# Optimization experiments

Hardware: AMD Instinct MI355X
Metric: run time of the kernel (lower is better)

## Reference

```python
import jax, jax.numpy as jnp
import numpy as np

B, T, OBS = 16, 4095, 128
HID, NH, FF, NL = 256, 8, 1024, 4
DH = HID // NH
ACT = 32
KEPS = 0.001   # performer kernel_epsilon (generalized attention default)
LNEPS = 1e-6   # flax LayerNorm default eps


def setup_inputs() -> dict:
    key = jax.random.key(0)
    ks = list(jax.random.split(key, 16))
    s = 0.02
    r = lambda k, shape: jax.random.normal(k, shape, jnp.float32) * s
    return {
        "hidden_state": jnp.zeros((B, 1, HID), jnp.float32),
        "ins": jax.random.normal(ks[0], (B, T, OBS), jnp.float32),
        "resets": jax.random.randint(ks[1], (B,), 0, 2).astype(bool),
        "emb_W": r(ks[2], (OBS, HID)), "emb_b": jnp.zeros((HID,), jnp.float32),
        "Wq": r(ks[3], (NL, HID, NH, DH)), "bq": jnp.zeros((NL, NH, DH), jnp.float32),
        "Wk": r(ks[4], (NL, HID, NH, DH)), "bk": jnp.zeros((NL, NH, DH), jnp.float32),
        "Wv": r(ks[5], (NL, HID, NH, DH)), "bv": jnp.zeros((NL, NH, DH), jnp.float32),
        "Wo": r(ks[6], (NL, NH, DH, HID)), "bo": jnp.zeros((NL, HID), jnp.float32),
        "ln1_s": jnp.ones((NL, HID), jnp.float32), "ln1_b": jnp.zeros((NL, HID), jnp.float32),
        "W1": r(ks[7], (NL, HID, FF)), "b1": jnp.zeros((NL, FF), jnp.float32),
        "W2": r(ks[8], (NL, FF, HID)), "b2": jnp.zeros((NL, HID), jnp.float32),
        "ln2_s": jnp.ones((NL, HID), jnp.float32), "ln2_b": jnp.zeros((NL, HID), jnp.float32),
        "qp_W": r(ks[9], (HID, ACT)), "qp_b": jnp.zeros((ACT,), jnp.float32),
    }


def layer_norm(x, scale, bias):
    m = x.mean(-1, keepdims=True)
    v = ((x - m) ** 2).mean(-1, keepdims=True)
    return (x - m) * jax.lax.rsqrt(v + LNEPS) * scale + bias


def favor_attention(q, k, v):
    # FAVOR+ generalized attention with deterministic relu features (no random
    # projection, make_fast_generalized_attention defaults), bidirectional,
    # renormalized. q,k,v: [B, L, H, Dh]; feature dim M == Dh.
    qp = jax.nn.relu(q) + KEPS
    kp = jax.nn.relu(k) + KEPS
    kv = jnp.einsum('blhm,blhd->bhmd', kp, v)            # [B,H,M,Dh]
    num = jnp.einsum('blhm,bhmd->blhd', qp, kv)           # [B,L,H,Dh]
    den = jnp.einsum('blhm,bhm->blh', qp, kp.sum(axis=1))  # [B,L,H]
    return num / den[..., None]


def encoder_block(x, Wq, bq, Wk, bk, Wv, bv, Wo, bo, ln1_s, ln1_b, W1, b1, W2, b2, ln2_s, ln2_b):
    q = jnp.einsum('bld,dhm->blhm', x, Wq) + bq
    k = jnp.einsum('bld,dhm->blhm', x, Wk) + bk
    v = jnp.einsum('bld,dhm->blhm', x, Wv) + bv
    a = favor_attention(q, k, v)
    o = jnp.einsum('blhm,hmd->bld', a, Wo) + bo
    x = o + o  # faithful to source: x = attn(x); x = x + dropout(x)
    x = layer_norm(x, ln1_s, ln1_b)
    h = jax.nn.relu(x @ W1 + b1) @ W2 + b2
    h = h + h  # same residual quirk on the FFN branch
    return layer_norm(h, ln2_s, ln2_b)


def reference(hidden_state, ins, resets, emb_W, emb_b, Wq, bq, Wk, bk, Wv, bv, Wo, bo, ln1_s, ln1_b, W1, b1, W2, b2, ln2_s, ln2_b, qp_W, qp_b):
    emb = ins @ emb_W + emb_b                         # [B, T, HID]
    hs = jnp.where(resets[:, None, None], 0.0, hidden_state)
    x = jnp.concatenate([hs, emb], axis=-2)           # [B, 1+T, HID]
    for i in range(NL):
        x = encoder_block(x, Wq[i], bq[i], Wk[i], bk[i], Wv[i], bv[i], Wo[i], bo[i],
                          ln1_s[i], ln1_b[i], W1[i], b1[i], W2[i], b2[i], ln2_s[i], ln2_b[i])
    new_hidden = x[..., 0:1, :]                       # carry token
    q_vals = new_hidden @ qp_W + qp_b                 # [B, 1, ACT]
    return new_hidden, q_vals
```

## Files before the change

kernel.cpp:

```cpp
#include <hip/hip_runtime.h>


typedef unsigned short bf16_t;
typedef __attribute__((ext_vector_type(8))) short short8;
typedef __attribute__((ext_vector_type(4))) float float4v;

#define NB 16
#define LSEQ 4096
#define MROWS (NB * LSEQ)
#define HIDD 256
#define NHEAD 8
#define DHEAD 32
#define FFD 1024
#define NLAY 4
#define KEPS_F 1e-3f
#define LNEPS_F 1e-6f
#define KV_ELEMS (NB * NHEAD * 32 * 33)

__device__ __forceinline__ float b2f(bf16_t h) {
    return __uint_as_float(((unsigned int)h) << 16);
}
__device__ __forceinline__ bf16_t f2b(float f) {
    unsigned int u = __float_as_uint(f);
    u += 0x7fffu + ((u >> 16) & 1u);
    return (bf16_t)(u >> 16);
}

#define GLOAD_LDS16(g, l)                                                     \
    __builtin_amdgcn_global_load_lds(                                         \
        (const __attribute__((address_space(1))) void*)(g),                   \
        (__attribute__((address_space(3))) void*)(l), 16, 0, 0)

#define SBAR() __builtin_amdgcn_s_barrier()
#define WAITV(n)                                                              \
    do {                                                                      \
        asm volatile("s_waitcnt vmcnt(" #n ")" ::: "memory");                 \
        __builtin_amdgcn_sched_barrier(0);                                    \
    } while (0)

#define FRAG16(L, R)                                                          \
    (*(const short8*)&(L)[((((R) >> 1) * 8) +                                  \
        (((((R) & 1) << 2) | quad) ^ (((R) >> 1) & 7))) * 8])

__global__ __launch_bounds__(256) void conv_transpose_kernel(
    const float* __restrict__ in, bf16_t* __restrict__ out, int R, int C,
    size_t ils, size_t ols)
{
    __shared__ float tile[32][33];
    const size_t ib = (size_t)blockIdx.z * ils;
    const size_t ob = (size_t)blockIdx.z * ols;
    const int r0 = blockIdx.y * 32, c0 = blockIdx.x * 32;
    const int tx = threadIdx.x & 31, ty = threadIdx.x >> 5;
#pragma unroll
    for (int rr = ty; rr < 32; rr += 8)
        tile[rr][tx] = in[ib + (size_t)(r0 + rr) * C + c0 + tx];
    __syncthreads();
#pragma unroll
    for (int rr = ty; rr < 32; rr += 8)
        out[ob + (size_t)(c0 + rr) * R + r0 + tx] = f2b(tile[tx][rr]);
}

__global__ __launch_bounds__(256) void concat_bias_kernel(
    const float* __restrict__ bq, const float* __restrict__ bk,
    const float* __restrict__ bv, float* __restrict__ bqkv)
{
    const int l = blockIdx.x, j = threadIdx.x;
    bqkv[l * 768 + j]       = bq[l * 256 + j];
    bqkv[l * 768 + 256 + j] = bk[l * 256 + j];
    bqkv[l * 768 + 512 + j] = bv[l * 256 + j];
}

__global__ __launch_bounds__(256) void prep_a_kernel(
    const float* __restrict__ ins, bf16_t* __restrict__ Ain)
{
    const int row = blockIdx.x * 2 + (threadIdx.x >> 7);
    const int j = threadIdx.x & 127;
    const int b = row >> 12, l = row & (LSEQ - 1);
    bf16_t v = 0;
    if (l != 0) v = f2b(ins[((size_t)b * 4095 + (l - 1)) * 128 + j]);
    Ain[(size_t)row * 128 + j] = v;
}

__global__ __launch_bounds__(256) void fix_row0_kernel(
    const float* __restrict__ hidden, const int* __restrict__ resets,
    bf16_t* __restrict__ X)
{
    const int b = blockIdx.x, j = threadIdx.x;
    float v = resets[b] ? 0.f : hidden[b * HIDD + j];
    X[((size_t)b * LSEQ) * HIDD + j] = f2b(v);
}

template <int MODE>
__global__ __launch_bounds__(512, 4) void gemm_pipe(
    const bf16_t* __restrict__ A, const bf16_t* __restrict__ WT,
    const float* __restrict__ bias, bf16_t* __restrict__ C,
    int M, int N, int K, int lda, int ldc)
{
    __shared__ __align__(16) bf16_t As[3][128 * 32];
    __shared__ __align__(16) bf16_t Bs[3][256 * 32];

    const int tid = threadIdx.x;
    const int wave = tid >> 6, lane = tid & 63;
    const int quad = lane >> 4, mr = lane & 15;

    const int Nn = N >> 8;
    const int id = blockIdx.x;
    const int s = id >> 3;
    const int bm = (((id & 7) + ((s / Nn) << 3))) << 7;
    const int bn = (s % Nn) << 8;

    const int wm = (wave & 1) << 6;
    const int wn = (wave >> 1) << 6;

    const int KT = K >> 5;

    float bcol[4];
#pragma unroll
    for (int j = 0; j < 4; ++j) bcol[j] = bias[bn + wn + j * 16 + mr];
    asm volatile("s_waitcnt vmcnt(0)" ::: "memory");
    __builtin_amdgcn_sched_barrier(0);

    auto stageA = [&](int t) {
        const int k0 = t << 5;
        bf16_t* L = &As[t % 3][0];
        const int c = tid;
        const int r = c >> 2;
        const int up = ((((r & 1) << 2) | (c & 3)) ^ ((r >> 1) & 7));
        const int grow = ((r >> 1) << 1) | (up >> 2);
        GLOAD_LDS16(A + (size_t)(bm + grow) * lda + k0 + ((up & 3) << 3),
                    L + c * 8);
    };
    auto stageB = [&](int t) {
        const int k0 = t << 5;
        bf16_t* L = &Bs[t % 3][0];
#pragma unroll
        for (int it = 0; it < 2; ++it) {
            const int c = it * 512 + tid;
            const int r = c >> 2;
            const int up = ((((r & 1) << 2) | (c & 3)) ^ ((r >> 1) & 7));
            const int grow = ((r >> 1) << 1) | (up >> 2);
            GLOAD_LDS16(WT + (size_t)(bn + grow) * K + k0 + ((up & 3) << 3),
                        L + c * 8);
        }
    };

    float4v acc[4][4];
#pragma unroll
    for (int i = 0; i < 4; i++)
#pragma unroll
        for (int j = 0; j < 4; j++) acc[i][j] = (float4v)(0.f);

    const int P = KT < 2 ? KT : 2;
    for (int tt = 0; tt < P; ++tt) { stageA(tt); stageB(tt); }

    for (int t = 0; t < KT; ++t) {
        if (t < KT - 1) { WAITV(3); } else { WAITV(0); }
        SBAR();
        __builtin_amdgcn_sched_barrier(0);
        if (t + 2 < KT) { stageA(t + 2); stageB(t + 2); }
        const bf16_t* LA = &As[t % 3][0];
        const bf16_t* LB = &Bs[t % 3][0];
        short8 a[4], b[4];
#pragma unroll
        for (int j = 0; j < 4; ++j) b[j] = FRAG16(LB, wn + j * 16 + mr);
#pragma unroll
        for (int i = 0; i < 4; ++i) a[i] = FRAG16(LA, wm + i * 16 + mr);
        __builtin_amdgcn_s_setprio(1);
        __builtin_amdgcn_sched_barrier(0);
#pragma unroll
        for (int i = 0; i < 4; ++i)
#pragma unroll
            for (int j = 0; j < 4; ++j)
                acc[i][j] = __builtin_amdgcn_mfma_f32_16x16x32_bf16(
                    a[i], b[j], acc[i][j], 0, 0, 0);
        __builtin_amdgcn_sched_barrier(0);
        __builtin_amdgcn_s_setprio(0);
    }

#pragma unroll
    for (int i = 0; i < 4; ++i) {
#pragma unroll
        for (int r = 0; r < 4; ++r) {
            const int grow = bm + wm + i * 16 + quad * 4 + r;
            bf16_t* crow = C + (size_t)grow * ldc + bn + wn + mr;
#pragma unroll
            for (int j = 0; j < 4; ++j) {
                float v = acc[i][j][r] + bcol[j];
                if (MODE == 1) v = fmaxf(v, 0.f);
                crow[j * 16] = f2b(v);
            }
        }
    }
}

__global__ __launch_bounds__(512, 4) void gemm_ln_pipe(
    const bf16_t* __restrict__ A, const bf16_t* __restrict__ WT,
    const float* __restrict__ bias, const float* __restrict__ sc,
    const float* __restrict__ bi, bf16_t* __restrict__ out,
    int K, int lda)
{
    __shared__ __align__(16) bf16_t As[3][128 * 32];
    __shared__ __align__(16) bf16_t Bs[3][256 * 32];
    __shared__ float red[8][64][2];
    __shared__ float fin[128][2];

    const int tid = threadIdx.x;
    const int wave = tid >> 6, lane = tid & 63;
    const int quad = lane >> 4, mr = lane & 15;
    const int bm = blockIdx.x << 7;

    const int wm = (wave & 1) << 6;
    const int wn = (wave >> 1) << 6;

    const int KT = K >> 5;

    float bcol[4], scv[4], biv[4];
#pragma unroll
    for (int j = 0; j < 4; ++j) {
        bcol[j] = bias[wn + j * 16 + mr];
        scv[j]  = sc[wn + j * 16 + mr];
        biv[j]  = bi[wn + j * 16 + mr];
    }
    asm volatile("s_waitcnt vmcnt(0)" ::: "memory");
    __builtin_amdgcn_sched_barrier(0);

    auto stageA = [&](int t) {
        const int k0 = t << 5;
        bf16_t* L = &As[t % 3][0];
        const int c = tid;
        const int r = c >> 2;
        const int up = ((((r & 1) << 2) | (c & 3)) ^ ((r >> 1) & 7));
        const int grow = ((r >> 1) << 1) | (up >> 2);
        GLOAD_LDS16(A + (size_t)(bm + grow) * lda + k0 + ((up & 3) << 3),
                    L + c * 8);
    };
    auto stageB = [&](int t) {
        const int k0 = t << 5;
        bf16_t* L = &Bs[t % 3][0];
#pragma unroll
        for (int it = 0; it < 2; ++it) {
            const int c = it * 512 + tid;
            const int r = c >> 2;
            const int up = ((((r & 1) << 2) | (c & 3)) ^ ((r >> 1) & 7));
            const int grow = ((r >> 1) << 1) | (up >> 2);
            GLOAD_LDS16(WT + (size_t)grow * K + k0 + ((up & 3) << 3),
                        L + c * 8);
        }
    };

    float4v acc[4][4];
#pragma unroll
    for (int i = 0; i < 4; i++)
#pragma unroll
        for (int j = 0; j < 4; j++) acc[i][j] = (float4v)(0.f);

    const int P = KT < 2 ? KT : 2;
    for (int tt = 0; tt < P; ++tt) { stageA(tt); stageB(tt); }

    for (int t = 0; t < KT; ++t) {
        if (t < KT - 1) { WAITV(3); } else { WAITV(0); }
        SBAR();
        __builtin_amdgcn_sched_barrier(0);
        if (t + 2 < KT) { stageA(t + 2); stageB(t + 2); }
        const bf16_t* LA = &As[t % 3][0];
        const bf16_t* LB = &Bs[t % 3][0];
        short8 a[4], b[4];
#pragma unroll
        for (int j = 0; j < 4; ++j) b[j] = FRAG16(LB, wn + j * 16 + mr);
#pragma unroll
        for (int i = 0; i < 4; ++i) a[i] = FRAG16(LA, wm + i * 16 + mr);
        __builtin_amdgcn_s_setprio(1);
        __builtin_amdgcn_sched_barrier(0);
#pragma unroll
        for (int i = 0; i < 4; ++i)
#pragma unroll
            for (int j = 0; j < 4; ++j)
                acc[i][j] = __builtin_amdgcn_mfma_f32_16x16x32_bf16(
                    a[i], b[j], acc[i][j], 0, 0, 0);
        __builtin_amdgcn_sched_barrier(0);
        __builtin_amdgcn_s_setprio(0);
    }

#pragma unroll
    for (int i = 0; i < 4; ++i) {
#pragma unroll
        for (int r = 0; r < 4; ++r) {
            float ss = 0.f, s2 = 0.f;
#pragma unroll
            for (int j = 0; j < 4; ++j) {
                const float v = 2.0f * (acc[i][j][r] + bcol[j]);
                ss += v; s2 += v * v;
            }
#pragma unroll
            for (int off = 1; off < 16; off <<= 1) {
                ss += __shfl_xor(ss, off, 64);
                s2 += __shfl_xor(s2, off, 64);
            }
            if (mr == 0) {
                const int rl = i * 16 + quad * 4 + r;
                red[wave][rl][0] = ss;
                red[wave][rl][1] = s2;
            }
        }
    }
    __syncthreads();
    if (tid < 256) {
        const int R = tid >> 1, p = tid & 1;
        const int mh = R >> 6, rl = R & 63;
        fin[R][p] = red[mh][rl][p] + red[mh + 2][rl][p]
                  + red[mh + 4][rl][p] + red[mh + 6][rl][p];
    }
    __syncthreads();

#pragma unroll
    for (int i = 0; i < 4; ++i) {
#pragma unroll
        for (int r = 0; r < 4; ++r) {
            const int R = wm + i * 16 + quad * 4 + r;
            const float mean = fin[R][0] * (1.0f / 256.0f);
            const float var  = fin[R][1] * (1.0f / 256.0f) - mean * mean;
            const float rs = rsqrtf(var + LNEPS_F);
            bf16_t* crow = out + (size_t)(bm + R) * 256 + wn + mr;
#pragma unroll
            for (int j = 0; j < 4; ++j) {
                const float v = 2.0f * (acc[i][j][r] + bcol[j]);
                crow[j * 16] = f2b((v - mean) * rs * scv[j] + biv[j]);
            }
        }
    }
}

__global__ __launch_bounds__(512) void favor_a_kernel(
    const bf16_t* __restrict__ QKV, const float* __restrict__ KV,
    bf16_t* __restrict__ Afav)
{
    __shared__ __align__(16) bf16_t kvT[NHEAD * 34 * 36];

    const int tid = threadIdx.x;
    const int wave = tid >> 6, lane = tid & 63;
    const int bm = blockIdx.x * 128;
    const int b = bm >> 12;
    const int quad = lane >> 4, mr = lane & 15;

    for (int e = tid; e < NHEAD * 34 * 32; e += 512) {
        const int h = e / (34 * 32);
        const int rem = e - h * (34 * 32);
        const int d = rem >> 5, m = rem & 31;
        bf16_t v = 0;
        if (d < 33) v = f2b(KV[((size_t)(b * NHEAD + h)) * (32 * 33) + m * 33 + d]);
        kvT[(h * 34 + d) * 36 + m] = v;
    }
    __syncthreads();

    const int Rrow = bm + wave * 16 + mr;
    const size_t abase = (size_t)(bm + wave * 16) * 256;

    short8 araw[NHEAD];
#pragma unroll
    for (int h = 0; h < NHEAD; ++h)
        araw[h] = *(const short8*)(QKV + (size_t)Rrow * 768 + h * 32 + quad * 8);

#pragma unroll
    for (int h = 0; h < NHEAD; ++h) {
        short8 a;
#pragma unroll
        for (int j = 0; j < 8; j++)
            a[j] = (short)f2b(fmaxf(b2f((bf16_t)araw[h][j]), 0.f) + KEPS_F);
        short8 bf0 = *(const short8*)&kvT[(h * 34 + mr) * 36 + quad * 8];
        short8 bf1 = *(const short8*)&kvT[(h * 34 + 16 + mr) * 36 + quad * 8];
        short8 bden;
#pragma unroll
        for (int j = 0; j < 8; j++) bden[j] = 0;
        if (mr == 0)
            bden = *(const short8*)&kvT[(h * 34 + 32) * 36 + quad * 8];
        float4v c0 = __builtin_amdgcn_mfma_f32_16x16x32_bf16(a, bf0, (float4v)(0.f), 0, 0, 0);
        float4v c1 = __builtin_amdgcn_mfma_f32_16x16x32_bf16(a, bf1, (float4v)(0.f), 0, 0, 0);
        float4v c2 = __builtin_amdgcn_mfma_f32_16x16x32_bf16(a, bden, (float4v)(0.f), 0, 0, 0);
#pragma unroll
        for (int r = 0; r < 4; r++) {
            const float den = __shfl(c2[r], quad << 4);
            const float rinv = 1.0f / den;
            const int rl = quad * 4 + r;
            Afav[abase + (size_t)rl * 256 + h * 32 + mr]      = f2b(c0[r] * rinv);
            Afav[abase + (size_t)rl * 256 + h * 32 + 16 + mr] = f2b(c1[r] * rinv);
        }
    }
}

__global__ __launch_bounds__(256) void zero_kv(float* __restrict__ KV)
{
    int i = blockIdx.x * 256 + threadIdx.x;
    if (i < KV_ELEMS) KV[i] = 0.f;
}

__global__ __launch_bounds__(256) void kv_mfma(
    const bf16_t* __restrict__ QKV, float* __restrict__ KV)
{
    __shared__ __align__(16) char smem[24576];
    bf16_t (*kp)[36] = (bf16_t(*)[36])smem;
    bf16_t (*vv)[52] = (bf16_t(*)[52])(smem + 9216);
    float (*red)[6][64][4] = (float(*)[6][64][4])smem;

    const int bh = blockIdx.x;
    const int b = bh >> 3, h = bh & 7;
    const size_t rowbase = (size_t)b * LSEQ + blockIdx.y * 512;
    const int tid = threadIdx.x;
    const int wave = tid >> 6, lane = tid & 63;
    const int quad = lane >> 4, mr = lane & 15;

    for (int e = tid; e < 128 * 20; e += 256) {
        const int l = e / 20, c = 32 + (e % 20);
        vv[l][c] = (c == 32) ? (bf16_t)0x3F80 : (bf16_t)0;
    }

    float4v acc[2][3];
#pragma unroll
    for (int i = 0; i < 2; i++)
#pragma unroll
        for (int t = 0; t < 3; t++) acc[i][t] = (float4v)(0.f);

    for (int pass = 0; pass < 4; pass++) {
        __syncthreads();
        const size_t lp = rowbase + pass * 128;
#pragma unroll
        for (int it = 0; it < 4; it++) {
            const int e = tid + it * 256;
            const int l = e >> 3, c0 = (e & 7) * 4;
            const bf16_t* src = QKV + (lp + l) * 768 + 256 + h * 32 + c0;
            ushort4 kq = *(const ushort4*)src;
            ushort4 vq = *(const ushort4*)(src + 256);
            ushort4 ko;
            ko.x = f2b(fmaxf(b2f(kq.x), 0.f) + KEPS_F);
            ko.y = f2b(fmaxf(b2f(kq.y), 0.f) + KEPS_F);
            ko.z = f2b(fmaxf(b2f(kq.z), 0.f) + KEPS_F);
            ko.w = f2b(fmaxf(b2f(kq.w), 0.f) + KEPS_F);
            *(ushort4*)&kp[l][c0] = ko;
            *(ushort4*)&vv[l][c0] = vq;
        }
        __syncthreads();

        const int lw = wave * 32 + quad * 8;
        short8 a[2], bb[3];
#pragma unroll
        for (int i = 0; i < 2; i++)
#pragma unroll
            for (int j = 0; j < 8; j++)
                a[i][j] = (short)kp[lw + j][i * 16 + mr];
#pragma unroll
        for (int t = 0; t < 3; t++)
#pragma unroll
            for (int j = 0; j < 8; j++)
                bb[t][j] = (short)vv[lw + j][t * 16 + mr];
#pragma unroll
        for (int i = 0; i < 2; i++)
#pragma unroll
            for (int t = 0; t < 3; t++)
                acc[i][t] = __builtin_amdgcn_mfma_f32_16x16x32_bf16(
                    a[i], bb[t], acc[i][t], 0, 0, 0);
    }

    __syncthreads();
#pragma unroll
    for (int i = 0; i < 2; i++)
#pragma unroll
        for (int t = 0; t < 3; t++)
#pragma unroll
            for (int r = 0; r < 4; r++)
                red[wave][i * 3 + t][lane][r] = acc[i][t][r];
    __syncthreads();

    float* dst = KV + (size_t)bh * (32 * 33);
    for (int e = tid; e < 6 * 64 * 4; e += 256) {
        const int t = e >> 8, li = (e >> 2) & 63, r = e & 3;
        const float s = red[0][t][li][r] + red[1][t][li][r]
                      + red[2][t][li][r] + red[3][t][li][r];
        const int i = t / 3, j = t % 3;
        const int m = i * 16 + (li >> 4) * 4 + r;
        const int d = j * 16 + (li & 15);
        if (d < 33) atomicAdd(&dst[m * 33 + d], s);
    }
}

__global__ __launch_bounds__(256) void head_kernel(
    const bf16_t* __restrict__ X, const float* __restrict__ qpW,
    const float* __restrict__ qpb, float* __restrict__ out)
{
    const int b = blockIdx.x, j = threadIdx.x;
    __shared__ float xr[HIDD];
    float v = b2f(X[((size_t)b * LSEQ) * HIDD + j]);
    xr[j] = v;
    out[b * HIDD + j] = v;
    __syncthreads();
    if (j < 32) {
        float acc = qpb[j];
        for (int d = 0; d < HIDD; d++)
            acc = fmaf(xr[d], qpW[d * 32 + j], acc);
        out[NB * HIDD + b * 32 + j] = acc;
    }
}

extern "C" void kernel_launch(void* const* d_in, const int* in_sizes, int n_in,
                              void* d_out, int out_size, void* d_ws, size_t ws_size,
                              hipStream_t stream)
{
    const float* hidden = (const float*)d_in[0];
    const float* ins    = (const float*)d_in[1];
    const int*   resets = (const int*)d_in[2];
    const float* embW   = (const float*)d_in[3];
    const float* embb   = (const float*)d_in[4];
    const float* Wq = (const float*)d_in[5];
    const float* bq = (const float*)d_in[6];
    const float* Wk = (const float*)d_in[7];
    const float* bk = (const float*)d_in[8];
    const float* Wv = (const float*)d_in[9];
    const float* bv = (const float*)d_in[10];
    const float* Wo = (const float*)d_in[11];
    const float* bo = (const float*)d_in[12];
    const float* ln1s = (const float*)d_in[13];
    const float* ln1b = (const float*)d_in[14];
    const float* W1 = (const float*)d_in[15];
    const float* b1 = (const float*)d_in[16];
    const float* W2 = (const float*)d_in[17];
    const float* b2 = (const float*)d_in[18];
    const float* ln2s = (const float*)d_in[19];
    const float* ln2b = (const float*)d_in[20];
    const float* qpW = (const float*)d_in[21];
    const float* qpb = (const float*)d_in[22];

    const size_t ACT_SZ = (size_t)MROWS * HIDD;
    bf16_t* X    = (bf16_t*)d_ws;
    bf16_t* QKV  = X + ACT_SZ;
    bf16_t* H1   = QKV;
    bf16_t* Ain  = QKV;
    bf16_t* Afav = QKV + (size_t)MROWS * 768;
    float*  KV   = (float*)(QKV + (size_t)MROWS * FFD);
    float*  bqkv = KV + KV_ELEMS;
    bf16_t* WqkvT = (bf16_t*)(bqkv + NLAY * 768);
    bf16_t* WoT   = WqkvT + (size_t)NLAY * 3 * HIDD * HIDD;
    bf16_t* W1T   = WoT + (size_t)NLAY * HIDD * HIDD;
    bf16_t* W2T   = W1T + (size_t)NLAY * HIDD * FFD;
    bf16_t* embWT = W2T + (size_t)NLAY * FFD * HIDD;

    const dim3 blk(256);
    const dim3 blk512(512);
    const size_t HH = (size_t)HIDD * HIDD;

    conv_transpose_kernel<<<dim3(8, 8, NLAY), blk, 0, stream>>>(Wq, WqkvT,          HIDD, HIDD, HH, 3 * HH);
    conv_transpose_kernel<<<dim3(8, 8, NLAY), blk, 0, stream>>>(Wk, WqkvT + HH,     HIDD, HIDD, HH, 3 * HH);
    conv_transpose_kernel<<<dim3(8, 8, NLAY), blk, 0, stream>>>(Wv, WqkvT + 2 * HH, HIDD, HIDD, HH, 3 * HH);
    conv_transpose_kernel<<<dim3(8, 8, NLAY), blk, 0, stream>>>(Wo, WoT, HIDD, HIDD, HH, HH);
    conv_transpose_kernel<<<dim3(32, 8, NLAY), blk, 0, stream>>>(W1, W1T, HIDD, FFD, (size_t)HIDD * FFD, (size_t)HIDD * FFD);
    conv_transpose_kernel<<<dim3(8, 32, NLAY), blk, 0, stream>>>(W2, W2T, FFD, HIDD, (size_t)HIDD * FFD, (size_t)HIDD * FFD);
    conv_transpose_kernel<<<dim3(8, 4, 1), blk, 0, stream>>>(embW, embWT, 128, HIDD, 0, 0);
    concat_bias_kernel<<<NLAY, blk, 0, stream>>>(bq, bk, bv, bqkv);

    prep_a_kernel<<<MROWS / 2, blk, 0, stream>>>(ins, Ain);
    gemm_pipe<0><<<dim3(512), blk512, 0, stream>>>(Ain, embWT, embb, X, MROWS, HIDD, 128, 128, HIDD);
    fix_row0_kernel<<<NB, blk, 0, stream>>>(hidden, resets, X);

    for (int l = 0; l < NLAY; l++) {
        gemm_pipe<0><<<dim3(512 * 3), blk512, 0, stream>>>(X, WqkvT + (size_t)l * 3 * HH,
                                                           bqkv + l * 768, QKV, MROWS, 768, HIDD, HIDD, 768);

        zero_kv<<<(KV_ELEMS + 255) / 256, blk, 0, stream>>>(KV);
        kv_mfma<<<dim3(NB * NHEAD, 8), blk, 0, stream>>>(QKV, KV);

        favor_a_kernel<<<dim3(MROWS / 128), blk512, 0, stream>>>(QKV, KV, Afav);

        gemm_ln_pipe<<<dim3(512), blk512, 0, stream>>>(
            Afav, WoT + (size_t)l * HH, bo + l * HIDD,
            ln1s + l * HIDD, ln1b + l * HIDD, X, HIDD, HIDD);

        gemm_pipe<1><<<dim3(512 * 4), blk512, 0, stream>>>(X, W1T + (size_t)l * HIDD * FFD,
                                                           b1 + l * FFD, H1, MROWS, FFD, HIDD, HIDD, FFD);
        gemm_ln_pipe<<<dim3(512), blk512, 0, stream>>>(
            H1, W2T + (size_t)l * FFD * HIDD, b2 + l * HIDD,
            ln2s + l * HIDD, ln2b + l * HIDD, X, FFD, FFD);
    }

    head_kernel<<<NB, blk, 0, stream>>>(X, qpW, qpb, (float*)d_out);
}
```

Before: 1.016 ms.

## Double GEMM M-tile to 256 rows and move prefetch after fragment loads

All GEMM kernels now compute 256x256 output tiles instead of 128x256, giving each wave 128x64 of output through a second set of A fragments and twice the accumulators. This halves the number of blocks and reuses each B tile across twice as many rows, cutting B loads from global memory and LDS. The next-stage prefetch is issued after the LDS fragment reads, and the wait count is adjusted for the extra A load. The cost is higher register and LDS use, occupancy lowered to 2 blocks per CU, and as few as 256 blocks for the narrow GEMMs, which may underfill the GPU.

```diff
diff --git a/kernel.cpp b/kernel.cpp
--- a/kernel.cpp
+++ b/kernel.cpp
@@ -91,12 +91,12 @@
 }
 
 template <int MODE>
-__global__ __launch_bounds__(512, 4) void gemm_pipe(
+__global__ __launch_bounds__(512, 2) void gemm_pipe2(
     const bf16_t* __restrict__ A, const bf16_t* __restrict__ WT,
     const float* __restrict__ bias, bf16_t* __restrict__ C,
     int M, int N, int K, int lda, int ldc)
 {
-    __shared__ __align__(16) bf16_t As[3][128 * 32];
+    __shared__ __align__(16) bf16_t As[3][256 * 32];
     __shared__ __align__(16) bf16_t Bs[3][256 * 32];
 
     const int tid = threadIdx.x;
@@ -106,10 +106,10 @@
     const int Nn = N >> 8;
     const int id = blockIdx.x;
     const int s = id >> 3;
-    const int bm = (((id & 7) + ((s / Nn) << 3))) << 7;
+    const int bm = (((id & 7) + ((s / Nn) << 3))) << 8;
     const int bn = (s % Nn) << 8;
 
-    const int wm = (wave & 1) << 6;
+    const int wm = (wave & 1) << 7;
     const int wn = (wave >> 1) << 6;
 
     const int KT = K >> 5;
@@ -123,12 +123,15 @@
     auto stageA = [&](int t) {
         const int k0 = t << 5;
         bf16_t* L = &As[t % 3][0];
-        const int c = tid;
-        const int r = c >> 2;
-        const int up = ((((r & 1) << 2) | (c & 3)) ^ ((r >> 1) & 7));
-        const int grow = ((r >> 1) << 1) | (up >> 2);
-        GLOAD_LDS16(A + (size_t)(bm + grow) * lda + k0 + ((up & 3) << 3),
-                    L + c * 8);
+#pragma unroll
+        for (int it = 0; it < 2; ++it) {
+            const int c = it * 512 + tid;
+            const int r = c >> 2;
+            const int up = ((((r & 1) << 2) | (c & 3)) ^ ((r >> 1) & 7));
+            const int grow = ((r >> 1) << 1) | (up >> 2);
+            GLOAD_LDS16(A + (size_t)(bm + grow) * lda + k0 + ((up & 3) << 3),
+                        L + c * 8);
+        }
     };
     auto stageB = [&](int t) {
         const int k0 = t << 5;
@@ -144,9 +147,9 @@
         }
     };
 
-    float4v acc[4][4];
-#pragma unroll
-    for (int i = 0; i < 4; i++)
+    float4v acc[8][4];
+#pragma unroll
+    for (int i = 0; i < 8; i++)
 #pragma unroll
         for (int j = 0; j < 4; j++) acc[i][j] = (float4v)(0.f);
 
@@ -154,17 +157,19 @@
     for (int tt = 0; tt < P; ++tt) { stageA(tt); stageB(tt); }
 
     for (int t = 0; t < KT; ++t) {
-        if (t < KT - 1) { WAITV(3); } else { WAITV(0); }
+        if (t < KT - 1) { WAITV(4); } else { WAITV(0); }
         SBAR();
         __builtin_amdgcn_sched_barrier(0);
-        if (t + 2 < KT) { stageA(t + 2); stageB(t + 2); }
         const bf16_t* LA = &As[t % 3][0];
         const bf16_t* LB = &Bs[t % 3][0];
-        short8 a[4], b[4];
-#pragma unroll
-        for (int j = 0; j < 4; ++j) b[j] = FRAG16(LB, wn + j * 16 + mr);
-#pragma unroll
-        for (int i = 0; i < 4; ++i) a[i] = FRAG16(LA, wm + i * 16 + mr);
+        short8 a0[4], a1[4], b[4];
+#pragma unroll
+        for (int j = 0; j < 4; ++j) b[j]  = FRAG16(LB, wn + j * 16 + mr);
+#pragma unroll
+        for (int i = 0; i < 4; ++i) a0[i] = FRAG16(LA, wm + i * 16 + mr);
+#pragma unroll
+        for (int i = 0; i < 4; ++i) a1[i] = FRAG16(LA, wm + 64 + i * 16 + mr);
+        if (t + 2 < KT) { stageA(t + 2); stageB(t + 2); }
         __builtin_amdgcn_s_setprio(1);
         __builtin_amdgcn_sched_barrier(0);
 #pragma unroll
@@ -172,13 +177,19 @@
 #pragma unroll
             for (int j = 0; j < 4; ++j)
                 acc[i][j] = __builtin_amdgcn_mfma_f32_16x16x32_bf16(
-                    a[i], b[j], acc[i][j], 0, 0, 0);
+                    a0[i], b[j], acc[i][j], 0, 0, 0);
+#pragma unroll
+        for (int i = 0; i < 4; ++i)
+#pragma unroll
+            for (int j = 0; j < 4; ++j)
+                acc[4 + i][j] = __builtin_amdgcn_mfma_f32_16x16x32_bf16(
+                    a1[i], b[j], acc[4 + i][j], 0, 0, 0);
         __builtin_amdgcn_sched_barrier(0);
         __builtin_amdgcn_s_setprio(0);
     }
 
 #pragma unroll
-    for (int i = 0; i < 4; ++i) {
+    for (int i = 0; i < 8; ++i) {
 #pragma unroll
         for (int r = 0; r < 4; ++r) {
             const int grow = bm + wm + i * 16 + quad * 4 + r;
@@ -193,23 +204,23 @@
     }
 }
 
-__global__ __launch_bounds__(512, 4) void gemm_ln_pipe(
+__global__ __launch_bounds__(512, 2) void gemm_pipe2_ln(
     const bf16_t* __restrict__ A, const bf16_t* __restrict__ WT,
     const float* __restrict__ bias, const float* __restrict__ sc,
     const float* __restrict__ bi, bf16_t* __restrict__ out,
     int K, int lda)
 {
-    __shared__ __align__(16) bf16_t As[3][128 * 32];
+    __shared__ __align__(16) bf16_t As[3][256 * 32];
     __shared__ __align__(16) bf16_t Bs[3][256 * 32];
-    __shared__ float red[8][64][2];
-    __shared__ float fin[128][2];
+    __shared__ float red[8][128][2];
+    __shared__ float fin[256][2];
 
     const int tid = threadIdx.x;
     const int wave = tid >> 6, lane = tid & 63;
     const int quad = lane >> 4, mr = lane & 15;
-    const int bm = blockIdx.x << 7;
-
-    const int wm = (wave & 1) << 6;
+    const int bm = blockIdx.x << 8;
+
+    const int wm = (wave & 1) << 7;
     const int wn = (wave >> 1) << 6;
 
     const int KT = K >> 5;
@@ -227,12 +238,15 @@
     auto stageA = [&](int t) {
         const int k0 = t << 5;
         bf16_t* L = &As[t % 3][0];
-        const int c = tid;
-        const int r = c >> 2;
-        const int up = ((((r & 1) << 2) | (c & 3)) ^ ((r >> 1) & 7));
-        const int grow = ((r >> 1) << 1) | (up >> 2);
-        GLOAD_LDS16(A + (size_t)(bm + grow) * lda + k0 + ((up & 3) << 3),
-                    L + c * 8);
+#pragma unroll
+        for (int it = 0; it < 2; ++it) {
+            const int c = it * 512 + tid;
+            const int r = c >> 2;
+            const int up = ((((r & 1) << 2) | (c & 3)) ^ ((r >> 1) & 7));
+            const int grow = ((r >> 1) << 1) | (up >> 2);
+            GLOAD_LDS16(A + (size_t)(bm + grow) * lda + k0 + ((up & 3) << 3),
+                        L + c * 8);
+        }
     };
     auto stageB = [&](int t) {
         const int k0 = t << 5;
@@ -248,9 +262,9 @@
         }
     };
 
-    float4v acc[4][4];
-#pragma unroll
-    for (int i = 0; i < 4; i++)
+    float4v acc[8][4];
+#pragma unroll
+    for (int i = 0; i < 8; i++)
 #pragma unroll
         for (int j = 0; j < 4; j++) acc[i][j] = (float4v)(0.f);
 
@@ -258,17 +272,19 @@
     for (int tt = 0; tt < P; ++tt) { stageA(tt); stageB(tt); }
 
     for (int t = 0; t < KT; ++t) {
-        if (t < KT - 1) { WAITV(3); } else { WAITV(0); }
+        if (t < KT - 1) { WAITV(4); } else { WAITV(0); }
         SBAR();
         __builtin_amdgcn_sched_barrier(0);
-        if (t + 2 < KT) { stageA(t + 2); stageB(t + 2); }
         const bf16_t* LA = &As[t % 3][0];
         const bf16_t* LB = &Bs[t % 3][0];
-        short8 a[4], b[4];
-#pragma unroll
-        for (int j = 0; j < 4; ++j) b[j] = FRAG16(LB, wn + j * 16 + mr);
-#pragma unroll
-        for (int i = 0; i < 4; ++i) a[i] = FRAG16(LA, wm + i * 16 + mr);
+        short8 a0[4], a1[4], b[4];
+#pragma unroll
+        for (int j = 0; j < 4; ++j) b[j]  = FRAG16(LB, wn + j * 16 + mr);
+#pragma unroll
+        for (int i = 0; i < 4; ++i) a0[i] = FRAG16(LA, wm + i * 16 + mr);
+#pragma unroll
+        for (int i = 0; i < 4; ++i) a1[i] = FRAG16(LA, wm + 64 + i * 16 + mr);
+        if (t + 2 < KT) { stageA(t + 2); stageB(t + 2); }
         __builtin_amdgcn_s_setprio(1);
         __builtin_amdgcn_sched_barrier(0);
 #pragma unroll
@@ -276,13 +292,19 @@
 #pragma unroll
             for (int j = 0; j < 4; ++j)
                 acc[i][j] = __builtin_amdgcn_mfma_f32_16x16x32_bf16(
-                    a[i], b[j], acc[i][j], 0, 0, 0);
+                    a0[i], b[j], acc[i][j], 0, 0, 0);
+#pragma unroll
+        for (int i = 0; i < 4; ++i)
+#pragma unroll
+            for (int j = 0; j < 4; ++j)
+                acc[4 + i][j] = __builtin_amdgcn_mfma_f32_16x16x32_bf16(
+                    a1[i], b[j], acc[4 + i][j], 0, 0, 0);
         __builtin_amdgcn_sched_barrier(0);
         __builtin_amdgcn_s_setprio(0);
     }
 
 #pragma unroll
-    for (int i = 0; i < 4; ++i) {
+    for (int i = 0; i < 8; ++i) {
 #pragma unroll
         for (int r = 0; r < 4; ++r) {
             float ss = 0.f, s2 = 0.f;
@@ -304,16 +326,16 @@
         }
     }
     __syncthreads();
-    if (tid < 256) {
+    {
         const int R = tid >> 1, p = tid & 1;
-        const int mh = R >> 6, rl = R & 63;
+        const int mh = R >> 7, rl = R & 127;
         fin[R][p] = red[mh][rl][p] + red[mh + 2][rl][p]
                   + red[mh + 4][rl][p] + red[mh + 6][rl][p];
     }
     __syncthreads();
 
 #pragma unroll
-    for (int i = 0; i < 4; ++i) {
+    for (int i = 0; i < 8; ++i) {
 #pragma unroll
         for (int r = 0; r < 4; ++r) {
             const int R = wm + i * 16 + quad * 4 + r;
@@ -555,25 +577,25 @@
     concat_bias_kernel<<<NLAY, blk, 0, stream>>>(bq, bk, bv, bqkv);
 
     prep_a_kernel<<<MROWS / 2, blk, 0, stream>>>(ins, Ain);
-    gemm_pipe<0><<<dim3(512), blk512, 0, stream>>>(Ain, embWT, embb, X, MROWS, HIDD, 128, 128, HIDD);
+    gemm_pipe2<0><<<dim3(256), blk512, 0, stream>>>(Ain, embWT, embb, X, MROWS, HIDD, 128, 128, HIDD);
     fix_row0_kernel<<<NB, blk, 0, stream>>>(hidden, resets, X);
 
     for (int l = 0; l < NLAY; l++) {
-        gemm_pipe<0><<<dim3(512 * 3), blk512, 0, stream>>>(X, WqkvT + (size_t)l * 3 * HH,
-                                                           bqkv + l * 768, QKV, MROWS, 768, HIDD, HIDD, 768);
+        gemm_pipe2<0><<<dim3(256 * 3), blk512, 0, stream>>>(X, WqkvT + (size_t)l * 3 * HH,
+                                                            bqkv + l * 768, QKV, MROWS, 768, HIDD, HIDD, 768);
 
         zero_kv<<<(KV_ELEMS + 255) / 256, blk, 0, stream>>>(KV);
         kv_mfma<<<dim3(NB * NHEAD, 8), blk, 0, stream>>>(QKV, KV);
 
         favor_a_kernel<<<dim3(MROWS / 128), blk512, 0, stream>>>(QKV, KV, Afav);
 
-        gemm_ln_pipe<<<dim3(512), blk512, 0, stream>>>(
+        gemm_pipe2_ln<<<dim3(256), blk512, 0, stream>>>(
             Afav, WoT + (size_t)l * HH, bo + l * HIDD,
             ln1s + l * HIDD, ln1b + l * HIDD, X, HIDD, HIDD);
 
-        gemm_pipe<1><<<dim3(512 * 4), blk512, 0, stream>>>(X, W1T + (size_t)l * HIDD * FFD,
-                                                           b1 + l * FFD, H1, MROWS, FFD, HIDD, HIDD, FFD);
-        gemm_ln_pipe<<<dim3(512), blk512, 0, stream>>>(
+        gemm_pipe2<1><<<dim3(256 * 4), blk512, 0, stream>>>(X, W1T + (size_t)l * HIDD * FFD,
+                                                            b1 + l * FFD, H1, MROWS, FFD, HIDD, HIDD, FFD);
+        gemm_pipe2_ln<<<dim3(256), blk512, 0, stream>>>(
             H1, W2T + (size_t)l * FFD * HIDD, b2 + l * HIDD,
             ln2s + l * HIDD, ln2b + l * HIDD, X, FFD, FFD);
     }
```

Measured after the change: 1.002 ms. No clear change (-1.4%).
